# Optimization experiments

Measured on AMD Instinct MI355X. Metric: run time of the kernel, lower is better.

Reference implementation:

```python
import jax, jax.numpy as jnp
import numpy as np

NUM_NODES = 100000
NUM_EDGES = 3200000
N_PER = 400            # nodes per graph (equal-size graphs)
NUM_GRAPHS = 250
K = 100                # sort-pooling k
DIM = 32
IN_DIM = 128
TOTAL = 3 * DIM + 1    # 97 = concat channel count
GDIM = 128
OUT_DIM = 2
DENSE_DIM = (((K - 2) // 2 + 1) - 5 + 1) * 64  # 46*64 = 2944


def setup_inputs() -> dict:
    key = jax.random.key(0)
    ks = jax.random.split(key, 12)

    def lin(k, shape, fan_in):
        return jax.random.normal(k, shape, jnp.float32) / np.float32(np.sqrt(fan_in))

    return {
        "x": jax.random.normal(ks[0], (NUM_NODES, IN_DIM), jnp.float32),
        "edge_index": jax.random.randint(ks[1], (2, NUM_EDGES), 0, NUM_NODES, dtype=jnp.int32),
        "batch": jnp.arange(NUM_NODES, dtype=jnp.int32) // N_PER,
        "W1": lin(ks[2], (IN_DIM, DIM), IN_DIM), "b1": jnp.zeros((DIM,), jnp.float32),
        "W2": lin(ks[3], (DIM, DIM), DIM),       "b2": jnp.zeros((DIM,), jnp.float32),
        "W3": lin(ks[4], (DIM, DIM), DIM),       "b3": jnp.zeros((DIM,), jnp.float32),
        "W4": lin(ks[5], (DIM, 1), DIM),         "b4": jnp.zeros((1,), jnp.float32),
        "cw1": lin(ks[6], (128, 1, TOTAL), TOTAL),   "cb1": jnp.zeros((128,), jnp.float32),
        "cw2": lin(ks[7], (64, 128, 5), 128 * 5),    "cb2": jnp.zeros((64,), jnp.float32),
        "fw1": lin(ks[8], (GDIM, DENSE_DIM), DENSE_DIM), "fb1": jnp.zeros((GDIM,), jnp.float32),
        "fw3": lin(ks[9], (OUT_DIM, GDIM), GDIM),        "fb3": jnp.zeros((OUT_DIM,), jnp.float32),
    }


def _gcn(h_in, W, b, src, dst, coef, deg_inv):
    # GCNConv (improved=False): D^{-1/2}(A+I)D^{-1/2} (h W) + b
    h = h_in @ W
    agg = jax.ops.segment_sum(h[src] * coef, dst, num_segments=NUM_NODES)
    return agg + h * deg_inv[:, None] + b  # deg_inv = self-loop norm dis[i]^2


def reference(x, edge_index, batch, W1, b1, W2, b2, W3, b3, W4, b4,
              cw1, cb1, cw2, cb2, fw1, fb1, fw3, fb3):
    src, dst = edge_index[0], edge_index[1]
    deg = jax.ops.segment_sum(jnp.ones((NUM_EDGES,), x.dtype), dst, num_segments=NUM_NODES) + 1.0
    dis = jax.lax.rsqrt(deg)
    coef = (dis[src] * dis[dst])[:, None]
    deg_inv = 1.0 / deg

    x1 = jnp.tanh(_gcn(x,  W1, b1, src, dst, coef, deg_inv))
    x2 = jnp.tanh(_gcn(x1, W2, b2, src, dst, coef, deg_inv))
    x3 = jnp.tanh(_gcn(x2, W3, b3, src, dst, coef, deg_inv))
    x4 = jnp.tanh(_gcn(x2, W4, b4, src, dst, coef, deg_inv))  # NB: conv4 consumes x2 (as in source)
    xc = jnp.concatenate([x1, x2, x3, x4], axis=1)  # [N, 97]

    # global_sort_pool: per-graph descending sort by last channel, keep top K nodes
    order = jnp.lexsort((-xc[:, -1], batch))  # primary: graph id, secondary: -last channel
    xs = xc[order].reshape(NUM_GRAPHS, N_PER, TOTAL)[:, :K]  # [B, K, 97]

    # Conv1d(1, 128, kernel=stride=97) over flattened [B,1,K*97] == per-slot linear map
    c1 = jax.nn.relu(jnp.einsum('bkt,ct->bck', xs, cw1[:, 0, :]) + cb1[None, :, None])  # [B,128,K]
    p1 = c1.reshape(NUM_GRAPHS, 128, K // 2, 2).max(axis=-1)  # MaxPool1d(2,2) -> [B,128,50]
    c2 = jax.lax.conv_general_dilated(p1, cw2, (1,), 'VALID',
                                      dimension_numbers=('NCH', 'OIH', 'NCH'))
    c2 = jax.nn.relu(c2 + cb2[None, :, None])  # [B,64,46]

    flat = c2.reshape(NUM_GRAPHS, -1)            # [B, 2944]
    h = jax.nn.relu(flat @ fw1.T + fb1)          # fc1 + relu (dropout = identity in eval)
    logits = h @ fw3.T + fb3                     # fc3
    return jax.nn.log_softmax(logits, axis=-1)
```

## Files before the change

kernel.cpp:

```cpp
#include <hip/hip_runtime.h>
#include <hip/hip_bf16.h>

#define NNODES 100000
#define NEDGES 3200000
#define NPADE  4000000
#define NPER   400
#define NGRAPH 250
#define KTOP   100
#define DIM    32
#define INDIM  128
#define TOTALC 97
#define BSHIFT 7
#define BNODES 128
#define NBUCK  782
#define NCHUNK 200
#define CHSZ   16000

__device__ __forceinline__ float bf(unsigned short u) {
    return __uint_as_float(((unsigned)u) << 16);
}
__device__ __forceinline__ unsigned short f2bf(float f) {
    unsigned u = __float_as_uint(f);
    unsigned r = ((u >> 16) & 1u) + 0x7FFFu;
    return (unsigned short)((u + r) >> 16);
}

#define OW_W1   0
#define OW_B1   4096
#define OW_W2   4128
#define OW_B2   5152
#define OW_W3   5184
#define OW_B3   6208
#define OW_W4   6240
#define OW_B4   6272
#define OW_CW1  6280
#define OW_CB1  18696
#define OW_CW2  18824
#define OW_CB2  59784
#define OW_FW1  59848
#define OW_FB1  436680
#define OW_FW3  436808
#define OW_FB3  437064
#define OW_TOT  437072


__global__ void k_detect(const unsigned int* __restrict__ xw, int* __restrict__ flag) {
    __shared__ int cnt[256];
    int t = threadIdx.x, c = 0;
    for (int i = t; i < 4096; i += 256) {
        unsigned e = (xw[i] >> 23) & 0xFFu;
        if (e >= 100u && e <= 150u) c++;
    }
    cnt[t] = c;
    __syncthreads();
    for (int off = 128; off > 0; off >>= 1) {
        if (t < off) cnt[t] += cnt[t + off];
        __syncthreads();
    }
    if (t == 0) flag[0] = (cnt[0] < 2048) ? 1 : 0;
}

struct Srcs { const void* p[16]; };

__global__ void k_convert(Srcs sr, float* __restrict__ dst, const int* __restrict__ flag) {
    const int st[16] = {OW_W1, OW_B1, OW_W2, OW_B2, OW_W3, OW_B3, OW_W4, OW_B4,
                        OW_CW1, OW_CB1, OW_CW2, OW_CB2, OW_FW1, OW_FB1, OW_FW3, OW_FB3};
    const int nn[16] = {4096, 32, 1024, 32, 1024, 32, 32, 1,
                        12416, 128, 40960, 64, 376832, 128, 256, 2};
    int idx = blockIdx.x * 256 + threadIdx.x;
    if (idx >= OW_TOT) return;
    int isb = flag[0];
    #pragma unroll
    for (int s = 0; s < 16; s++) {
        if (idx >= st[s] && idx < st[s] + nn[s]) {
            int l = idx - st[s];
            dst[idx] = isb ? bf(((const unsigned short*)sr.p[s])[l])
                           : ((const float*)sr.p[s])[l];
        }
    }
}

__global__ void k_w1t(const float* __restrict__ fw1f, float* __restrict__ fw1t) {
    int i = blockIdx.x * 256 + threadIdx.x;
    if (i < 376832) {
        int j = i / 2944, d = i % 2944;
        fw1t[d * 128 + j] = fw1f[i];
    }
}


__global__ __launch_bounds__(1024) void k_hist(const int* __restrict__ ei, int* __restrict__ ghist) {
    __shared__ int h[NBUCK];
    int c = blockIdx.x, t = threadIdx.x;
    for (int i = t; i < NBUCK; i += 1024) h[i] = 0;
    __syncthreads();
    int base = c * CHSZ;
    for (int e = base + t; e < base + CHSZ; e += 1024)
        atomicAdd(&h[ei[NEDGES + e] >> BSHIFT], 1);
    __syncthreads();
    for (int i = t; i < NBUCK; i += 1024) ghist[i * NCHUNK + c] = h[i];
}

__global__ __launch_bounds__(256) void k_scanChunk(int* __restrict__ ghist, int* __restrict__ bcnt) {
    __shared__ int s[256];
    int b = blockIdx.x, t = threadIdx.x;
    int v = (t < NCHUNK) ? ghist[b * NCHUNK + t] : 0;
    s[t] = v;
    __syncthreads();
    for (int o = 1; o < 256; o <<= 1) {
        int u = (t >= o) ? s[t - o] : 0;
        __syncthreads();
        s[t] += u;
        __syncthreads();
    }
    if (t < NCHUNK) ghist[b * NCHUNK + t] = s[t] - v;
    if (t == NCHUNK - 1) bcnt[b] = s[t];
}

__global__ void k_scanB(const int* __restrict__ bcnt, int* __restrict__ boff) {
    __shared__ int s[1024];
    int t = threadIdx.x;
    int v = (t < NBUCK) ? bcnt[t] : 0;
    s[t] = v;
    __syncthreads();
    for (int o = 1; o < 1024; o <<= 1) {
        int u = (t >= o) ? s[t - o] : 0;
        __syncthreads();
        s[t] += u;
        __syncthreads();
    }
    if (t < NBUCK) boff[t] = s[t] - v;
}

__global__ __launch_bounds__(1024) void k_binwrite(const int* __restrict__ ei, const int* __restrict__ boff,
                           const int* __restrict__ ghist, unsigned* __restrict__ staged) {
    __shared__ int cur[NBUCK];
    int c = blockIdx.x, t = threadIdx.x;
    for (int i = t; i < NBUCK; i += 1024) cur[i] = boff[i] + ghist[i * NCHUNK + c];
    __syncthreads();
    int base = c * CHSZ;
    for (int e = base + t; e < base + CHSZ; e += 1024) {
        int s = ei[e], d = ei[NEDGES + e];
        int b = d >> BSHIFT;
        int pos = atomicAdd(&cur[b], 1);
        staged[pos] = ((unsigned)(d & (BNODES - 1)) << 17) | (unsigned)s;
    }
}

__global__ __launch_bounds__(256) void k_nodecnt(const unsigned* __restrict__ staged,
                          const int* __restrict__ boff, int* __restrict__ degi) {
    __shared__ int cnt[BNODES];
    int b = blockIdx.x, t = threadIdx.x;
    if (t < BNODES) cnt[t] = 0;
    __syncthreads();
    int s0 = boff[b];
    int s1 = (b + 1 < NBUCK) ? boff[b + 1] : NEDGES;
    for (int i = s0 + t; i < s1; i += 256)
        atomicAdd(&cnt[staged[i] >> 17], 1);
    __syncthreads();
    int n0 = b << BSHIFT;
    int nn = min(BNODES, NNODES - n0);
    if (t < nn) degi[n0 + t] = cnt[t];
}

__global__ void k_nodeprep(const int* __restrict__ degi, float* __restrict__ dis,
                           float* __restrict__ dinv) {
    int i = blockIdx.x * 256 + threadIdx.x;
    if (i < NNODES) {
        float d = (float)(degi[i] + 1);
        dis[i]  = rsqrtf(d);
        dinv[i] = 1.0f / d;
    }
}

__global__ void k_bsum(const int* __restrict__ degi, int* __restrict__ bsums) {
    __shared__ int s[256];
    int t = threadIdx.x;
    int i = blockIdx.x * 256 + t;
    s[t] = (i < NNODES) ? ((degi[i] + 7) & ~7) : 0;
    __syncthreads();
    for (int off = 128; off > 0; off >>= 1) {
        if (t < off) s[t] += s[t + off];
        __syncthreads();
    }
    if (t == 0) bsums[blockIdx.x] = s[0];
}

__global__ void k_scanb(int* __restrict__ bsums, int nb) {
    __shared__ int s[512];
    int t = threadIdx.x;
    int v = (t < nb) ? bsums[t] : 0;
    s[t] = v;
    __syncthreads();
    for (int off = 1; off < 512; off <<= 1) {
        int u = (t >= off) ? s[t - off] : 0;
        __syncthreads();
        s[t] += u;
        __syncthreads();
    }
    if (t < nb) bsums[t] = s[t] - v;
}

__global__ void k_scanf(const int* __restrict__ degi, const int* __restrict__ bsums,
                        int* __restrict__ row_off) {
    __shared__ int s[256];
    int t = threadIdx.x;
    int i = blockIdx.x * 256 + t;
    int v = (i < NNODES) ? ((degi[i] + 7) & ~7) : 0;
    s[t] = v;
    __syncthreads();
    for (int off = 1; off < 256; off <<= 1) {
        int u = (t >= off) ? s[t - off] : 0;
        __syncthreads();
        s[t] += u;
        __syncthreads();
    }
    if (i < NNODES) row_off[i] = bsums[blockIdx.x] + s[t] - v;
}

__global__ __launch_bounds__(256) void k_csrfix(const unsigned* __restrict__ staged,
                         const int* __restrict__ boff, const int* __restrict__ row_off,
                         const float* __restrict__ dis,
                         int* __restrict__ csr_src, float* __restrict__ csr_cf) {
    __shared__ int cnt[BNODES];
    __shared__ int rofs[BNODES];
    __shared__ float disl[BNODES];
    int b = blockIdx.x, t = threadIdx.x;
    int n0 = b << BSHIFT;
    int nn = min(BNODES, NNODES - n0);
    if (t < BNODES) {
        cnt[t]  = 0;
        rofs[t] = (t < nn) ? row_off[n0 + t] : 0;
        disl[t] = (t < nn) ? dis[n0 + t] : 0.f;
    }
    __syncthreads();
    int s0 = boff[b];
    int s1 = (b + 1 < NBUCK) ? boff[b + 1] : NEDGES;
    for (int i = s0 + t; i < s1; i += 256) {
        unsigned rec = staged[i];
        int dl = rec >> 17, s = rec & 0x1FFFF;
        int r = atomicAdd(&cnt[dl], 1);
        int slot = rofs[dl] + r;
        csr_src[slot] = s;
        csr_cf[slot]  = dis[s] * disl[dl];
    }
    __syncthreads();
    if (t < nn) {
        int d = cnt[t], dp = (d + 7) & ~7;
        for (int s2 = d; s2 < dp; s2++) {
            csr_src[rofs[t] + s2] = 0;
            csr_cf[rofs[t] + s2]  = 0.f;
        }
    }
}


__global__ void k_mm1(const void* __restrict__ xraw, const float* __restrict__ W1f,
                      const int* __restrict__ flag, float* __restrict__ h) {
    __shared__ float w[INDIM * DIM];
    __shared__ float xsh[8 * INDIM];
    int t = threadIdx.x;
    for (int i = t; i < INDIM * DIM; i += 256) w[i] = W1f[i];
    if (flag[0]) {
        const unsigned int* xsrc = (const unsigned int*)((const unsigned short*)xraw
                                   + (size_t)blockIdx.x * 8 * INDIM);
        for (int i = t; i < 512; i += 256) {
            unsigned u = xsrc[i];
            xsh[2 * i]     = __uint_as_float(u << 16);
            xsh[2 * i + 1] = __uint_as_float(u & 0xFFFF0000u);
        }
    } else {
        const float4* xsrc = (const float4*)((const float*)xraw + (size_t)blockIdx.x * 8 * INDIM);
        float4* xdst = (float4*)xsh;
        for (int i = t; i < 256; i += 256) xdst[i] = xsrc[i];
    }
    __syncthreads();
    int ln = t >> 5, c = t & 31;
    const float* xr = xsh + ln * INDIM;
    float acc = 0.f;
    #pragma unroll 8
    for (int j = 0; j < INDIM; j++) acc += xr[j] * w[j * DIM + c];
    h[(size_t)blockIdx.x * 256 + t] = acc;
}

__global__ void k_mm32(const float* __restrict__ xin, const float* __restrict__ W,
                       const float* __restrict__ W4, float* __restrict__ h,
                       float* __restrict__ h4) {
    __shared__ float w[DIM * DIM];
    __shared__ float w4s[DIM];
    __shared__ float xsh[8 * DIM];
    int t = threadIdx.x;
    for (int i = t; i < DIM * DIM; i += 256) w[i] = W[i];
    if (W4 && t < DIM) w4s[t] = W4[t];
    for (int i = t; i < 8 * DIM; i += 256) xsh[i] = xin[(size_t)blockIdx.x * 256 + i];
    __syncthreads();
    int ln = t >> 5, c = t & 31;
    const float* xr = xsh + ln * DIM;
    float acc = 0.f;
    #pragma unroll
    for (int j = 0; j < DIM; j++) acc += xr[j] * w[j * DIM + c];
    h[(size_t)blockIdx.x * 256 + t] = acc;
    if (W4 && c == 0) {
        float a4 = 0.f;
        #pragma unroll
        for (int j = 0; j < DIM; j++) a4 += xr[j] * w4s[j];
        h4[blockIdx.x * 8 + ln] = a4;
    }
}

__global__ void k_gather(const float* __restrict__ h, const float* __restrict__ h4,
                         const int* __restrict__ csr_src, const float* __restrict__ csr_cf,
                         const int* __restrict__ row_off, const int* __restrict__ degi,
                         const float* __restrict__ dinv, const float* __restrict__ bias,
                         const float* __restrict__ b4,
                         float* __restrict__ xout, float* __restrict__ x4out) {
    int t = threadIdx.x;
    int node = blockIdx.x * 8 + (t >> 5);
    int lane = t & 31;
    int start = row_off[node];
    int cnt   = degi[node];
    int iters = (cnt + 7) >> 3;
    const int4*   ip = (const int4*)(csr_src + start);
    const float4* cp = (const float4*)(csr_cf + start);
    float acc0 = 0.f, acc1 = 0.f;
    if (iters > 0) {
        int4   iA = ip[0], iB = ip[1];
        float4 cA = cp[0], cB = cp[1];
        for (int k = 1; k < iters; k++) {
            int4   nA = ip[2 * k],     nB = ip[2 * k + 1];
            float4 dA = cp[2 * k],     dB = cp[2 * k + 1];
            acc0 += h[(size_t)iA.x * DIM + lane] * cA.x;
            acc1 += h[(size_t)iA.y * DIM + lane] * cA.y;
            acc0 += h[(size_t)iA.z * DIM + lane] * cA.z;
            acc1 += h[(size_t)iA.w * DIM + lane] * cA.w;
            acc0 += h[(size_t)iB.x * DIM + lane] * cB.x;
            acc1 += h[(size_t)iB.y * DIM + lane] * cB.y;
            acc0 += h[(size_t)iB.z * DIM + lane] * cB.z;
            acc1 += h[(size_t)iB.w * DIM + lane] * cB.w;
            iA = nA; iB = nB; cA = dA; cB = dB;
        }
        acc0 += h[(size_t)iA.x * DIM + lane] * cA.x;
        acc1 += h[(size_t)iA.y * DIM + lane] * cA.y;
        acc0 += h[(size_t)iA.z * DIM + lane] * cA.z;
        acc1 += h[(size_t)iA.w * DIM + lane] * cA.w;
        acc0 += h[(size_t)iB.x * DIM + lane] * cB.x;
        acc1 += h[(size_t)iB.y * DIM + lane] * cB.y;
        acc0 += h[(size_t)iB.z * DIM + lane] * cB.z;
        acc1 += h[(size_t)iB.w * DIM + lane] * cB.w;
    }
    float di = dinv[node];
    float outv = tanhf(acc0 + acc1 + h[(size_t)node * DIM + lane] * di + bias[lane]);
    xout[(size_t)node * DIM + lane] = outv;
    if (h4) {
        int cntp = iters << 3;
        float a4 = 0.f;
        for (int ee = lane; ee < cntp; ee += 32)
            a4 += h4[csr_src[start + ee]] * csr_cf[start + ee];
        for (int off = 16; off > 0; off >>= 1) a4 += __shfl_xor(a4, off, 32);
        if (lane == 0) x4out[node] = tanhf(a4 + h4[node] * di + b4[0]);
    }
}

__global__ void k_sortpool(const float* __restrict__ x4, int* __restrict__ sel) {
    __shared__ unsigned long long keys[512];
    int g = blockIdx.x, t = threadIdx.x;
    for (int i = t; i < 512; i += 256) {
        unsigned long long kk = 0xFFFFFFFFFFFFFFFFULL;
        if (i < NPER) {
            unsigned u = __float_as_uint(x4[g * NPER + i]);
            u = (u & 0x80000000u) ? ~u : (u | 0x80000000u);
            kk = ((unsigned long long)(~u) << 32) | (unsigned)i;
        }
        keys[i] = kk;
    }
    __syncthreads();
    for (int k = 2; k <= 512; k <<= 1)
        for (int j = k >> 1; j > 0; j >>= 1) {
            for (int i = t; i < 512; i += 256) {
                int l = i ^ j;
                if (l > i) {
                    unsigned long long a = keys[i], b = keys[l];
                    bool asc = ((i & k) == 0);
                    if ((a > b) == asc) { keys[i] = b; keys[l] = a; }
                }
            }
            __syncthreads();
        }
    for (int i = t; i < KTOP; i += 256)
        sel[g * KTOP + i] = g * NPER + (int)(unsigned)(keys[i] & 0xFFFFFFFFu);
}

__global__ __launch_bounds__(1024) void
k_conv1pool(const float* __restrict__ x1, const float* __restrict__ x2,
            const float* __restrict__ x3, const float* __restrict__ x4,
            const int* __restrict__ sel, const float* __restrict__ cw1f,
            const float* __restrict__ cb1f, float* __restrict__ p1g) {
    __shared__ __align__(16) float xs[32 * 100];
    __shared__ __align__(16) float ws[32 * 128];
    __shared__ int nsh[KTOP];
    int g = blockIdx.x, t = threadIdx.x;
    if (t < KTOP) nsh[t] = sel[g * KTOP + t];
    int ct = (t & 31) * 4;
    int kt = (t >> 5) * 4;
    bool act = (t < 800);
    float acc[4][4] = {};
    for (int ch = 0; ch < 3; ch++) {
        const float* arr = (ch == 0) ? x1 : (ch == 1) ? x2 : x3;
        __syncthreads();
        for (int i = t; i < 3200; i += 1024) {
            int q = i & 31, k = i >> 5;
            xs[q * 100 + k] = arr[(size_t)nsh[k] * 32 + q];
        }
        for (int i = t; i < 4096; i += 1024) {
            int c = i & 127, q = i >> 7;
            ws[q * 128 + c] = cw1f[c * TOTALC + ch * 32 + q];
        }
        __syncthreads();
        if (act) {
            for (int q = 0; q < 32; q++) {
                float4 wv = *(const float4*)&ws[q * 128 + ct];
                float4 xv = *(const float4*)&xs[q * 100 + kt];
                float xa[4] = { xv.x, xv.y, xv.z, xv.w };
                float wa[4] = { wv.x, wv.y, wv.z, wv.w };
                #pragma unroll
                for (int a = 0; a < 4; a++)
                    #pragma unroll
                    for (int b = 0; b < 4; b++)
                        acc[a][b] += xa[a] * wa[b];
            }
        }
    }
    if (act) {
        float wa[4];
        #pragma unroll
        for (int b = 0; b < 4; b++) wa[b] = cw1f[(ct + b) * TOTALC + 96];
        #pragma unroll
        for (int a = 0; a < 4; a++) {
            float xv = x4[nsh[kt + a]];
            #pragma unroll
            for (int b = 0; b < 4; b++) acc[a][b] += xv * wa[b];
        }
        int jbase = kt >> 1;
        #pragma unroll
        for (int b = 0; b < 4; b++) {
            float bias = cb1f[ct + b];
            float m0 = fmaxf(fmaxf(acc[0][b], acc[1][b]) + bias, 0.f);
            float m1 = fmaxf(fmaxf(acc[2][b], acc[3][b]) + bias, 0.f);
            p1g[((size_t)g * 128 + ct + b) * 50 + jbase]     = m0;
            p1g[((size_t)g * 128 + ct + b) * 50 + jbase + 1] = m1;
        }
    }
}

__global__ void k_w2t(const float* __restrict__ cw2f, float* __restrict__ w2t8) {
    int i = blockIdx.x * 256 + threadIdx.x;
    if (i < 64 * 128 * 8) {
        int q = i & 7;
        int co = i >> 3;
        int c = co >> 6, o = co & 63;
        w2t8[i] = (q < 5) ? cw2f[(o * 128 + c) * 5 + q] : 0.f;
    }
}

__global__ __launch_bounds__(1024) void
k_conv2fc(const float* __restrict__ p1g, const float* __restrict__ w2t8,
          const float* __restrict__ cb2f,
          const float* __restrict__ fw1t, const float* __restrict__ fb1f,
          const float* __restrict__ fw3f, const float* __restrict__ fb3f,
          const int* __restrict__ flag, void* __restrict__ outp) {
    __shared__ __align__(16) float p1s[128 * 52];
    __shared__ __align__(16) float flat[64 * 46];
    __shared__ __align__(16) float hp4[32 * 128];
    __shared__ float hsh[128];
    int g = blockIdx.x, t = threadIdx.x;
    for (int i = t; i < 128 * 50; i += 1024) {
        int c = i / 50, p = i % 50;
        p1s[c * 52 + p] = p1g[(size_t)g * 6400 + i];
    }
    for (int i = t; i < 128 * 2; i += 1024) {
        int c = i >> 1;
        p1s[c * 52 + 50 + (i & 1)] = 0.f;
    }
    for (int i = t; i < 2944; i += 1024) flat[i] = 0.f;
    __syncthreads();
    {
        int o = t & 63;
        int seg = t >> 6;
        int ph = seg & 1, c8 = seg >> 1;
        int p0 = ph ? 24 : 0;
        int np = ph ? 22 : 24;
        float acc[24];
        #pragma unroll
        for (int p = 0; p < 24; p++) acc[p] = 0.f;
        int cbeg = c8 * 16;
        for (int c = cbeg; c < cbeg + 16; c++) {
            const float4* wb = (const float4*)(w2t8 + (((size_t)c * 64 + o) << 3));
            float4 wA = wb[0], wB = wb[1];
            float w0 = wA.x, w1 = wA.y, w2 = wA.z, w3 = wA.w, w4 = wB.x;
            float win[28];
            const float4* wsrc = (const float4*)&p1s[c * 52 + p0];
            #pragma unroll
            for (int v = 0; v < 7; v++) {
                float4 f = wsrc[v];
                win[4 * v] = f.x; win[4 * v + 1] = f.y; win[4 * v + 2] = f.z; win[4 * v + 3] = f.w;
            }
            #pragma unroll
            for (int p = 0; p < 24; p++)
                acc[p] += win[p] * w0 + win[p + 1] * w1 + win[p + 2] * w2
                        + win[p + 3] * w3 + win[p + 4] * w4;
        }
        for (int p = 0; p < np; p++) atomicAdd(&flat[o * 46 + p0 + p], acc[p]);
    }
    __syncthreads();
    for (int i = t; i < 2944; i += 1024) {
        int o = i / 46;
        flat[i] = fmaxf(flat[i] + cb2f[o], 0.f);
    }
    __syncthreads();
    {
        int og = t & 31, slice = t >> 5;
        int d0 = slice * 92;
        const float4* flv = (const float4*)(flat + d0);
        const float4* wq  = (const float4*)fw1t + (size_t)d0 * 32 + og;
        float ax = 0.f, ay = 0.f, az = 0.f, aw = 0.f;
        #pragma unroll 2
        for (int j = 0; j < 23; j++) {
            float4 fv = flv[j];
            float4 w0 = wq[0], w1 = wq[32], w2 = wq[64], w3 = wq[96];
            ax += fv.x * w0.x + fv.y * w1.x + fv.z * w2.x + fv.w * w3.x;
            ay += fv.x * w0.y + fv.y * w1.y + fv.z * w2.y + fv.w * w3.y;
            az += fv.x * w0.z + fv.y * w1.z + fv.z * w2.z + fv.w * w3.z;
            aw += fv.x * w0.w + fv.y * w1.w + fv.z * w2.w + fv.w * w3.w;
            wq += 128;
        }
        float4* hp = (float4*)hp4 + slice * 32 + og;
        *hp = make_float4(ax, ay, az, aw);
    }
    __syncthreads();
    if (t < 128) {
        float s = fb1f[t];
        #pragma unroll 8
        for (int s2 = 0; s2 < 32; s2++) s += hp4[s2 * 128 + t];
        hsh[t] = fmaxf(s, 0.f);
    }
    __syncthreads();
    if (t < 64) {
        float h0 = hsh[t], h1 = hsh[t + 64];
        float l0 = h0 * fw3f[t] + h1 * fw3f[t + 64];
        float l1 = h0 * fw3f[128 + t] + h1 * fw3f[192 + t];
        #pragma unroll
        for (int off = 32; off > 0; off >>= 1) {
            l0 += __shfl_down(l0, off, 64);
            l1 += __shfl_down(l1, off, 64);
        }
        if (t == 0) {
            l0 += fb3f[0]; l1 += fb3f[1];
            float m = fmaxf(l0, l1);
            float lse = m + logf(expf(l0 - m) + expf(l1 - m));
            if (flag[0]) {
                unsigned short* ob = (unsigned short*)outp;
                ob[g * 2 + 0] = f2bf(l0 - lse);
                ob[g * 2 + 1] = f2bf(l1 - lse);
            } else {
                float* of = (float*)outp;
                of[g * 2 + 0] = l0 - lse;
                of[g * 2 + 1] = l1 - lse;
            }
        }
    }
}


extern "C" void kernel_launch(void* const* d_in, const int* in_sizes, int n_in,
                              void* d_out, int out_size, void* d_ws, size_t ws_size,
                              hipStream_t stream) {
    const void* x  = d_in[0];
    const int* ei  = (const int*)d_in[1];

    char* p = (char*)d_ws;
    auto alloc = [&](size_t bytes) -> void* {
        void* r = (void*)p;
        p += (bytes + 255) & ~(size_t)255;
        return r;
    };
    int*      flag    = (int*)alloc(256);
    float*    wcv     = (float*)alloc((size_t)OW_TOT * 4);
    float*    fw1t    = (float*)alloc((size_t)376832 * 4);
    int*      ghist   = (int*)alloc((size_t)NBUCK * NCHUNK * 4);
    int*      bcnt    = (int*)alloc(1024 * 4);
    int*      boff    = (int*)alloc(1024 * 4);
    int*      bsums   = (int*)alloc(512 * 4);
    int*      degi    = (int*)alloc((size_t)NNODES * 4);
    int*      row_off = (int*)alloc((size_t)NNODES * 4);
    float*    dis     = (float*)alloc((size_t)NNODES * 4);
    float*    dinv    = (float*)alloc((size_t)NNODES * 4);
    unsigned* staged  = (unsigned*)alloc((size_t)NEDGES * 4);
    int*      csr_src = (int*)alloc((size_t)NPADE * 4);
    float*    csr_cf  = (float*)alloc((size_t)NPADE * 4);
    float*    hbuf    = (float*)alloc((size_t)NNODES * DIM * 4);
    float*    h4buf   = (float*)alloc((size_t)NNODES * 4);
    float*    x1      = (float*)alloc((size_t)NNODES * DIM * 4);
    float*    x2      = (float*)alloc((size_t)NNODES * DIM * 4);
    float*    x3      = (float*)alloc((size_t)NNODES * DIM * 4);
    float*    x4      = (float*)alloc((size_t)NNODES * 4);
    int*      sel     = (int*)alloc((size_t)NGRAPH * KTOP * 4);
    float*    p1g     = (float*)alloc((size_t)NGRAPH * 128 * 50 * 4);
    float*    w2t     = (float*)alloc((size_t)64 * 128 * 8 * 4);
    (void)in_sizes; (void)n_in; (void)out_size; (void)ws_size;

    k_detect<<<1, 256, 0, stream>>>((const unsigned int*)x, flag);
    Srcs sr;
    for (int i = 0; i < 16; i++) sr.p[i] = d_in[3 + i];
    k_convert<<<(OW_TOT + 255) / 256, 256, 0, stream>>>(sr, wcv, flag);
    k_w1t    <<<1472, 256, 0, stream>>>(wcv + OW_FW1, fw1t);

    k_hist     <<<NCHUNK, 1024, 0, stream>>>(ei, ghist);
    k_scanChunk<<<NBUCK, 256, 0, stream>>>(ghist, bcnt);
    k_scanB    <<<1, 1024, 0, stream>>>(bcnt, boff);
    k_binwrite <<<NCHUNK, 1024, 0, stream>>>(ei, boff, ghist, staged);
    k_nodecnt  <<<NBUCK, 256, 0, stream>>>(staged, boff, degi);
    k_nodeprep <<<391, 256, 0, stream>>>(degi, dis, dinv);
    k_bsum     <<<391, 256, 0, stream>>>(degi, bsums);
    k_scanb    <<<1, 512, 0, stream>>>(bsums, 391);
    k_scanf    <<<391, 256, 0, stream>>>(degi, bsums, row_off);
    k_csrfix   <<<NBUCK, 256, 0, stream>>>(staged, boff, row_off, dis, csr_src, csr_cf);

    k_mm1   <<<12500, 256, 0, stream>>>(x, wcv + OW_W1, flag, hbuf);
    k_gather<<<12500, 256, 0, stream>>>(hbuf, nullptr, csr_src, csr_cf, row_off, degi, dinv,
                                        wcv + OW_B1, nullptr, x1, nullptr);
    k_mm32  <<<12500, 256, 0, stream>>>(x1, wcv + OW_W2, nullptr, hbuf, nullptr);
    k_gather<<<12500, 256, 0, stream>>>(hbuf, nullptr, csr_src, csr_cf, row_off, degi, dinv,
                                        wcv + OW_B2, nullptr, x2, nullptr);
    k_mm32  <<<12500, 256, 0, stream>>>(x2, wcv + OW_W3, wcv + OW_W4, hbuf, h4buf);
    k_gather<<<12500, 256, 0, stream>>>(hbuf, h4buf, csr_src, csr_cf, row_off, degi, dinv,
                                        wcv + OW_B3, wcv + OW_B4, x3, x4);

    k_sortpool <<<NGRAPH, 256, 0, stream>>>(x4, sel);
    k_conv1pool<<<NGRAPH, 1024, 0, stream>>>(x1, x2, x3, x4, sel, wcv + OW_CW1, wcv + OW_CB1, p1g);
    k_w2t      <<<256, 256, 0, stream>>>(wcv + OW_CW2, w2t);
    k_conv2fc  <<<NGRAPH, 1024, 0, stream>>>(p1g, w2t, wcv + OW_CB2, fw1t, wcv + OW_FB1,
                                             wcv + OW_FW3, wcv + OW_FB3, flag, d_out);
}
```

Before: 615.3 us.

## Split conv2/fc tail into three kernels with batched fc1 weight reuse

The fused per-graph conv2+fc1+fc3 kernel is split into three kernels. conv2 now runs two blocks per graph, one per output-position half, and writes the activations to global memory. fc1 is tiled so each block handles 5 graphs and one eighth of the input dimension, reusing each fc1 weight load across 5 graphs, and fc3 reduces the partial sums. This cuts redundant fc1 weight traffic, which was previously reread by every graph, and raises parallelism, at the cost of extra launches and global round-trips.

```diff
diff --git a/kernel.cpp b/kernel.cpp
--- a/kernel.cpp
+++ b/kernel.cpp
@@ -462,33 +462,29 @@
     }
 }
 
-__global__ __launch_bounds__(1024) void
-k_conv2fc(const float* __restrict__ p1g, const float* __restrict__ w2t8,
-          const float* __restrict__ cb2f,
-          const float* __restrict__ fw1t, const float* __restrict__ fb1f,
-          const float* __restrict__ fw3f, const float* __restrict__ fb3f,
-          const int* __restrict__ flag, void* __restrict__ outp) {
+__global__ __launch_bounds__(512) void
+k_conv2(const float* __restrict__ p1g, const float* __restrict__ w2t8,
+        const float* __restrict__ cb2f, float* __restrict__ flatg) {
     __shared__ __align__(16) float p1s[128 * 52];
-    __shared__ __align__(16) float flat[64 * 46];
-    __shared__ __align__(16) float hp4[32 * 128];
-    __shared__ float hsh[128];
-    int g = blockIdx.x, t = threadIdx.x;
-    for (int i = t; i < 128 * 50; i += 1024) {
+    __shared__ float fl[64 * 25];
+    int bid = blockIdx.x;
+    int g = bid >> 1, ph = bid & 1;
+    int t = threadIdx.x;
+    int p0 = ph ? 24 : 0;
+    int np = ph ? 22 : 24;
+    for (int i = t; i < 128 * 50; i += 512) {
         int c = i / 50, p = i % 50;
         p1s[c * 52 + p] = p1g[(size_t)g * 6400 + i];
     }
-    for (int i = t; i < 128 * 2; i += 1024) {
+    for (int i = t; i < 128 * 2; i += 512) {
         int c = i >> 1;
         p1s[c * 52 + 50 + (i & 1)] = 0.f;
     }
-    for (int i = t; i < 2944; i += 1024) flat[i] = 0.f;
+    for (int i = t; i < 64 * 25; i += 512) fl[i] = 0.f;
     __syncthreads();
     {
         int o = t & 63;
-        int seg = t >> 6;
-        int ph = seg & 1, c8 = seg >> 1;
-        int p0 = ph ? 24 : 0;
-        int np = ph ? 22 : 24;
+        int c8 = t >> 6;
         float acc[24];
         #pragma unroll
         for (int p = 0; p < 24; p++) acc[p] = 0.f;
@@ -509,40 +505,69 @@
                 acc[p] += win[p] * w0 + win[p + 1] * w1 + win[p + 2] * w2
                         + win[p + 3] * w3 + win[p + 4] * w4;
         }
-        for (int p = 0; p < np; p++) atomicAdd(&flat[o * 46 + p0 + p], acc[p]);
-    }
-    __syncthreads();
-    for (int i = t; i < 2944; i += 1024) {
-        int o = i / 46;
-        flat[i] = fmaxf(flat[i] + cb2f[o], 0.f);
-    }
-    __syncthreads();
-    {
-        int og = t & 31, slice = t >> 5;
-        int d0 = slice * 92;
-        const float4* flv = (const float4*)(flat + d0);
-        const float4* wq  = (const float4*)fw1t + (size_t)d0 * 32 + og;
-        float ax = 0.f, ay = 0.f, az = 0.f, aw = 0.f;
-        #pragma unroll 2
-        for (int j = 0; j < 23; j++) {
-            float4 fv = flv[j];
-            float4 w0 = wq[0], w1 = wq[32], w2 = wq[64], w3 = wq[96];
-            ax += fv.x * w0.x + fv.y * w1.x + fv.z * w2.x + fv.w * w3.x;
-            ay += fv.x * w0.y + fv.y * w1.y + fv.z * w2.y + fv.w * w3.y;
-            az += fv.x * w0.z + fv.y * w1.z + fv.z * w2.z + fv.w * w3.z;
-            aw += fv.x * w0.w + fv.y * w1.w + fv.z * w2.w + fv.w * w3.w;
-            wq += 128;
-        }
-        float4* hp = (float4*)hp4 + slice * 32 + og;
-        *hp = make_float4(ax, ay, az, aw);
-    }
-    __syncthreads();
-    if (t < 128) {
-        float s = fb1f[t];
-        #pragma unroll 8
-        for (int s2 = 0; s2 < 32; s2++) s += hp4[s2 * 128 + t];
-        hsh[t] = fmaxf(s, 0.f);
-    }
+        for (int p = 0; p < np; p++) atomicAdd(&fl[o * 25 + p], acc[p]);
+    }
+    __syncthreads();
+    for (int i = t; i < 64 * 24; i += 512) {
+        int o = i / 24, p = i - o * 24;
+        if (p < np)
+            flatg[(size_t)g * 2944 + o * 46 + p0 + p] = fmaxf(fl[o * 25 + p] + cb2f[o], 0.f);
+    }
+}
+
+__global__ __launch_bounds__(1024) void
+k_fc1(const float* __restrict__ flatg, const float* __restrict__ fw1t,
+      float* __restrict__ hpart) {
+    __shared__ float fls[5 * 368];
+    __shared__ float hp[8 * 5 * 128];
+    int b = blockIdx.x;
+    int gt = b >> 3, kt = b & 7;
+    int t = threadIdx.x;
+    int g0 = gt * 5;
+    int d0 = kt * 368;
+    for (int i = t; i < 5 * 368; i += 1024) {
+        int g = i / 368, dd = i - g * 368;
+        fls[i] = flatg[(size_t)(g0 + g) * 2944 + d0 + dd];
+    }
+    __syncthreads();
+    int og = t & 127, s8 = t >> 7;
+    int ds = s8 * 46;
+    const float* wp = fw1t + (size_t)(d0 + ds) * 128 + og;
+    const float* f0 = fls + ds;
+    float a0 = 0.f, a1 = 0.f, a2 = 0.f, a3 = 0.f, a4 = 0.f;
+    #pragma unroll 2
+    for (int d = 0; d < 46; d++) {
+        float w = wp[(size_t)d * 128];
+        a0 += f0[d]            * w;
+        a1 += f0[368 + d]      * w;
+        a2 += f0[2 * 368 + d]  * w;
+        a3 += f0[3 * 368 + d]  * w;
+        a4 += f0[4 * 368 + d]  * w;
+    }
+    hp[(s8 * 5 + 0) * 128 + og] = a0;
+    hp[(s8 * 5 + 1) * 128 + og] = a1;
+    hp[(s8 * 5 + 2) * 128 + og] = a2;
+    hp[(s8 * 5 + 3) * 128 + og] = a3;
+    hp[(s8 * 5 + 4) * 128 + og] = a4;
+    __syncthreads();
+    if (t < 640) {
+        int g = t >> 7, o2 = t & 127;
+        float s = 0.f;
+        #pragma unroll
+        for (int s2 = 0; s2 < 8; s2++) s += hp[(s2 * 5 + g) * 128 + o2];
+        hpart[((size_t)kt * NGRAPH + g0 + g) * 128 + o2] = s;
+    }
+}
+
+__global__ void k_fc3(const float* __restrict__ hpart, const float* __restrict__ fb1f,
+                      const float* __restrict__ fw3f, const float* __restrict__ fb3f,
+                      const int* __restrict__ flag, void* __restrict__ outp) {
+    __shared__ float hsh[128];
+    int g = blockIdx.x, t = threadIdx.x;
+    float s = fb1f[t];
+    #pragma unroll
+    for (int kt = 0; kt < 8; kt++) s += hpart[((size_t)kt * NGRAPH + g) * 128 + t];
+    hsh[t] = fmaxf(s, 0.f);
     __syncthreads();
     if (t < 64) {
         float h0 = hsh[t], h1 = hsh[t + 64];
@@ -606,6 +631,8 @@
     int*      sel     = (int*)alloc((size_t)NGRAPH * KTOP * 4);
     float*    p1g     = (float*)alloc((size_t)NGRAPH * 128 * 50 * 4);
     float*    w2t     = (float*)alloc((size_t)64 * 128 * 8 * 4);
+    float*    flatg   = (float*)alloc((size_t)NGRAPH * 2944 * 4);
+    float*    hpart   = (float*)alloc((size_t)8 * NGRAPH * 128 * 4);
     (void)in_sizes; (void)n_in; (void)out_size; (void)ws_size;
 
     k_detect<<<1, 256, 0, stream>>>((const unsigned int*)x, flag);
@@ -638,6 +665,8 @@
     k_sortpool <<<NGRAPH, 256, 0, stream>>>(x4, sel);
     k_conv1pool<<<NGRAPH, 1024, 0, stream>>>(x1, x2, x3, x4, sel, wcv + OW_CW1, wcv + OW_CB1, p1g);
     k_w2t      <<<256, 256, 0, stream>>>(wcv + OW_CW2, w2t);
-    k_conv2fc  <<<NGRAPH, 1024, 0, stream>>>(p1g, w2t, wcv + OW_CB2, fw1t, wcv + OW_FB1,
-                                             wcv + OW_FW3, wcv + OW_FB3, flag, d_out);
-}
+    k_conv2    <<<2 * NGRAPH, 512, 0, stream>>>(p1g, w2t, wcv + OW_CB2, flatg);
+    k_fc1      <<<400, 1024, 0, stream>>>(flatg, fw1t, hpart);
+    k_fc3      <<<NGRAPH, 128, 0, stream>>>(hpart, wcv + OW_FB1, wcv + OW_FW3, wcv + OW_FB3,
+                                            flag, d_out);
+}
```

After: 617.0 us. About the same (+0.3%).
